# Performance work log

Measured on AMD Instinct MI355X. Metric: run time of the kernel, lower is better.

Reference implementation:

```python
import jax, jax.numpy as jnp
import numpy as np

D_EMB = 1024
N_HEAD = 16
D_K = D_EMB // N_HEAD


def setup_inputs() -> dict:
    key = jax.random.key(0)
    ks = jax.random.split(key, 11)
    B, S = 2, 2048
    s = 1.0 / np.sqrt(D_EMB)
    inp = {
        'Q': jax.random.normal(ks[0], (B, S, D_EMB), jnp.float32),
        'K': jax.random.normal(ks[1], (B, S, D_EMB), jnp.float32),
        'V': jax.random.normal(ks[2], (B, S, D_EMB), jnp.float32),
        'W_Q': jax.random.normal(ks[3], (D_EMB, D_EMB), jnp.float32) * s,
        'b_Q': jax.random.normal(ks[4], (D_EMB,), jnp.float32) * s,
        'W_K': jax.random.normal(ks[5], (D_EMB, D_EMB), jnp.float32) * s,
        'b_K': jax.random.normal(ks[6], (D_EMB,), jnp.float32) * s,
        'W_V': jax.random.normal(ks[7], (D_EMB, D_EMB), jnp.float32) * s,
        'b_V': jax.random.normal(ks[8], (D_EMB,), jnp.float32) * s,
        'W_O': jax.random.normal(ks[9], (D_EMB, D_EMB), jnp.float32) * s,
        'b_O': jax.random.normal(ks[10], (D_EMB,), jnp.float32) * s,
    }
    return inp


def _heads(x):
    # [B, S, D] -> [B, H, S, d_k]
    B, S, _ = x.shape
    return x.reshape(B, S, N_HEAD, D_K).transpose(0, 2, 1, 3)


def reference(Q, K, V, W_Q, b_Q, W_K, b_K, W_V, b_V, W_O, b_O):
    q = _heads(Q @ W_Q.T + b_Q)
    k = _heads(K @ W_K.T + b_K)
    v = _heads(V @ W_V.T + b_V)
    scale = 1.0 / jnp.sqrt(jnp.asarray(D_K, q.dtype))
    scores = jnp.einsum('bhqd,bhkd->bhqk', q, k) * scale  # [B,H,S,S]
    probs = jax.nn.softmax(scores, axis=-1)
    attn = jnp.einsum('bhqk,bhkd->bhqd', probs, v)
    B, H, S, d = attn.shape
    attn = attn.transpose(0, 2, 1, 3).reshape(B, S, H * d)
    return attn @ W_O.T + b_O
```

## Files before the change

### kernel.cpp

```cpp
#include <hip/hip_runtime.h>
#include <cstdint>
#include <cstddef>

#define S_LEN 2048
#define NH    16
#define DKH   64
#define DEMB  1024
#define MTOT  4096

typedef float f32x4 __attribute__((ext_vector_type(4)));
typedef __bf16 bf16x8 __attribute__((ext_vector_type(8)));
typedef unsigned short u16;
typedef unsigned int u32;
typedef u16 u16x8 __attribute__((ext_vector_type(8)));
typedef u16 u16x4 __attribute__((ext_vector_type(4)));
typedef u32 u32x2 __attribute__((ext_vector_type(2)));

static __device__ __forceinline__ u16 f2bf(float f) {
  u32 u = __builtin_bit_cast(u32, f);
  u += 0x7fffu + ((u >> 16) & 1u);
  return (u16)(u >> 16);
}
static __device__ __forceinline__ float bf2f(u16 b) {
  return __builtin_bit_cast(float, ((u32)b) << 16);
}
static __device__ __forceinline__ bf16x8 ldfrag(const u16* p) {
  return __builtin_bit_cast(bf16x8, *(const u16x8*)p);
}
static __device__ __forceinline__ f32x4 mfma16(bf16x8 a, bf16x8 b, f32x4 c) {
  return __builtin_amdgcn_mfma_f32_16x16x32_bf16(a, b, c, 0, 0, 0);
}
static __device__ __forceinline__ void gl2lds16(const void* g, void* l) {
  __builtin_amdgcn_global_load_lds((__attribute__((address_space(1))) void*)g,
                                   (__attribute__((address_space(3))) void*)l,
                                   16, 0, 0);
}
static __device__ __forceinline__ u32 pkbf(float hi, float lo) {
  u32 a = __builtin_bit_cast(u32, hi) + 0x8000u;
  u32 b = __builtin_bit_cast(u32, lo) + 0x8000u;
  return __builtin_amdgcn_perm(a, b, 0x07060302u);
}

#define SCL_Q (0.125f * 1.44269504088896340736f)

__global__ __launch_bounds__(256) void cvt_bf16(const float* __restrict__ s,
                                                u16* __restrict__ d, int n) {
  int i = (blockIdx.x * 256 + threadIdx.x) * 4;
  if (i >= n) return;
  f32x4 f = *(const f32x4*)(s + i);
  u16x4 o;
  o[0] = f2bf(f[0]); o[1] = f2bf(f[1]); o[2] = f2bf(f[2]); o[3] = f2bf(f[3]);
  *(u16x4*)(d + i) = o;
}

__global__ __launch_bounds__(256) void qkv_gemm(
    const u16* __restrict__ qin, const u16* __restrict__ kin,
    const u16* __restrict__ vin, const u16* __restrict__ W,
    const float* __restrict__ bq, const float* __restrict__ bk,
    const float* __restrict__ bv,
    u16* __restrict__ qh, u16* __restrict__ kh, u16* __restrict__ vt) {
  __shared__ __align__(16) u16 sA[128 * 32];
  __shared__ __align__(16) u16 sB[128 * 32];
  const int t = threadIdx.x;
  const int l = t & 63, w = t >> 6;
  const int ll = l & 15, lg = l >> 4;
  const int nb = blockIdx.x;
  const int mb = blockIdx.y;
  const int which = nb >> 3;
  const u16* A = (which == 0) ? qin : ((which == 1) ? kin : vin);
  const int wr = (w >> 1) * 64, wc = (w & 1) * 64;

  f32x4 acc[4][4] = {};

  for (int kt = 0; kt < 32; ++kt) {
    const int k0 = kt * 32;
    __syncthreads();
#pragma unroll
    for (int i = 0; i < 2; ++i) {
      const int c = i * 256 + t;
      const int row = c >> 2;
      const int gc = (c & 3) ^ ((row >> 1) & 3);
      gl2lds16(A + (size_t)(mb * 128 + row) * DEMB + k0 + gc * 8, &sA[c * 8]);
      gl2lds16(W + (size_t)(nb * 128 + row) * DEMB + k0 + gc * 8, &sB[c * 8]);
    }
    __syncthreads();

    bf16x8 af[4], bfr[4];
#pragma unroll
    for (int i2 = 0; i2 < 4; ++i2) {
      const int row = wr + i2 * 16 + ll;
      af[i2] = ldfrag(&sA[row * 32 + (lg ^ ((row >> 1) & 3)) * 8]);
    }
#pragma unroll
    for (int j2 = 0; j2 < 4; ++j2) {
      const int row = wc + j2 * 16 + ll;
      bfr[j2] = ldfrag(&sB[row * 32 + (lg ^ ((row >> 1) & 3)) * 8]);
    }
#pragma unroll
    for (int i2 = 0; i2 < 4; ++i2)
#pragma unroll
      for (int j2 = 0; j2 < 4; ++j2)
        acc[i2][j2] = mfma16(af[i2], bfr[j2], acc[i2][j2]);
  }

  const float* bias = (which == 0) ? bq : ((which == 1) ? bk : bv);
  const int b = (mb * 128) >> 11;

  if (which == 2) {
#pragma unroll
    for (int j2 = 0; j2 < 4; ++j2) {
      const int nl = (nb * 128 + wc + j2 * 16 + ll) & 1023;
      const int h = nl >> 6, dk = nl & 63;
      const float bb = bias[nl];
      u16* base = vt + ((size_t)((b * NH + h) * DKH + dk)) * S_LEN;
#pragma unroll
      for (int i2 = 0; i2 < 4; ++i2) {
        const int s = (mb * 128 + wr + i2 * 16 + lg * 4) & 2047;
        u16x4 pk;
#pragma unroll
        for (int r = 0; r < 4; ++r) pk[r] = f2bf(acc[i2][j2][r] + bb);
        *(u16x4*)&base[s] = pk;
      }
    }
  } else {
    u16* outp = (which == 0) ? qh : kh;
    const float scl = (which == 0) ? SCL_Q : 1.0f;
#pragma unroll
    for (int j2 = 0; j2 < 4; ++j2) {
      const int nl = (nb * 128 + wc + j2 * 16 + ll) & 1023;
      const int h = nl >> 6, dk = nl & 63;
      const float bb = bias[nl];
#pragma unroll
      for (int i2 = 0; i2 < 4; ++i2) {
#pragma unroll
        for (int r = 0; r < 4; ++r) {
          const int s = (mb * 128 + wr + i2 * 16 + lg * 4 + r) & 2047;
          const float val = (acc[i2][j2][r] + bb) * scl;
          outp[((size_t)((b * NH + h) * S_LEN + s)) * DKH + dk] = f2bf(val);
        }
      }
    }
  }
}

__global__ __launch_bounds__(256) void attn_kernel(
    const u16* __restrict__ qh, const u16* __restrict__ kh,
    const u16* __restrict__ vt, u16* __restrict__ opart,
    float* __restrict__ lpart) {
  __shared__ __align__(16) u16 sK[64 * 64];
  __shared__ __align__(16) u16 sV[64 * 64];
  __shared__ __align__(16) u16 sP[4][2][16 * 68];
  const int t = threadIdx.x;
  const int l = t & 63, w = t >> 6;
  const int ll = l & 15, lg = l >> 4;
  const int qb = blockIdx.x >> 1;
  const int ks = blockIdx.x & 1;
  const int q_blk = qb * 128;
  const int bh = blockIdx.y;

  bf16x8 aq[2][2];
#pragma unroll
  for (int qt = 0; qt < 2; ++qt) {
    const u16* qbase = qh + ((size_t)bh * S_LEN + q_blk + w * 32 + qt * 16 + ll) * DKH;
    aq[qt][0] = ldfrag(qbase + lg * 8);
    aq[qt][1] = ldfrag(qbase + 32 + lg * 8);
  }

  f32x4 oT[2][4] = {};
  float l_part[2] = {0.f, 0.f};

  u16* sP0 = &sP[w][0][0];
  u16* sP1 = &sP[w][1][0];

  for (int kt = 0; kt < 16; ++kt) {
    const int kb0 = ks * 1024 + kt * 64;
    __syncthreads();
#pragma unroll
    for (int i = 0; i < 2; ++i) {
      const int c = i * 256 + t;
      const int row = c >> 3, gc = (c & 7) ^ (row & 7);
      gl2lds16(kh + ((size_t)bh * S_LEN + kb0 + row) * DKH + gc * 8,
               &sK[c * 8]);
      gl2lds16(vt + ((size_t)bh * DKH + row) * S_LEN + kb0 + gc * 8,
               &sV[c * 8]);
    }
    __syncthreads();

#pragma unroll
    for (int kbl = 0; kbl < 4; ++kbl) {
      const int krow = kbl * 16 + ll;
      const bf16x8 ak0 = ldfrag(&sK[krow * 64 + (lg ^ (ll & 7)) * 8]);
      const bf16x8 ak1 = ldfrag(&sK[krow * 64 + ((4 + lg) ^ (ll & 7)) * 8]);
      f32x4 s0 = {}, s1 = {};
      s0 = mfma16(ak0, aq[0][0], s0);
      s0 = mfma16(ak1, aq[0][1], s0);
      s1 = mfma16(ak0, aq[1][0], s1);
      s1 = mfma16(ak1, aq[1][1], s1);
      const int poff = ll * 68 + kbl * 16 + lg * 4;
      {
        const float p0 = __builtin_amdgcn_exp2f(s0[0]);
        const float p1 = __builtin_amdgcn_exp2f(s0[1]);
        const float p2 = __builtin_amdgcn_exp2f(s0[2]);
        const float p3 = __builtin_amdgcn_exp2f(s0[3]);
        l_part[0] += (p0 + p1) + (p2 + p3);
        u32x2 pk; pk[0] = pkbf(p1, p0); pk[1] = pkbf(p3, p2);
        *(u32x2*)&sP0[poff] = pk;
      }
      {
        const float p0 = __builtin_amdgcn_exp2f(s1[0]);
        const float p1 = __builtin_amdgcn_exp2f(s1[1]);
        const float p2 = __builtin_amdgcn_exp2f(s1[2]);
        const float p3 = __builtin_amdgcn_exp2f(s1[3]);
        l_part[1] += (p0 + p1) + (p2 + p3);
        u32x2 pk; pk[0] = pkbf(p1, p0); pk[1] = pkbf(p3, p2);
        *(u32x2*)&sP1[poff] = pk;
      }
    }

    bf16x8 bp[2][2];
#pragma unroll
    for (int fl = 0; fl < 2; ++fl) {
      const int off = ll * 68 + fl * 32 + lg * 8;
      const u16x4 lo0 = *(const u16x4*)&sP0[off];
      const u16x4 hi0 = *(const u16x4*)&sP0[off + 4];
      bp[0][fl] = __builtin_bit_cast(bf16x8,
          __builtin_shufflevector(lo0, hi0, 0, 1, 2, 3, 4, 5, 6, 7));
      const u16x4 lo1 = *(const u16x4*)&sP1[off];
      const u16x4 hi1 = *(const u16x4*)&sP1[off + 4];
      bp[1][fl] = __builtin_bit_cast(bf16x8,
          __builtin_shufflevector(lo1, hi1, 0, 1, 2, 3, 4, 5, 6, 7));
    }
#pragma unroll
    for (int nt = 0; nt < 4; ++nt) {
      const int vrow = nt * 16 + ll;
#pragma unroll
      for (int fl = 0; fl < 2; ++fl) {
        const bf16x8 av = ldfrag(&sV[vrow * 64 + ((fl * 4 + lg) ^ (vrow & 7)) * 8]);
        oT[0][nt] = mfma16(av, bp[0][fl], oT[0][nt]);
        oT[1][nt] = mfma16(av, bp[1][fl], oT[1][nt]);
      }
    }
  }

#pragma unroll
  for (int qt = 0; qt < 2; ++qt) {
    float lv = l_part[qt];
    lv += __shfl_xor(lv, 16, 64);
    lv += __shfl_xor(lv, 32, 64);
    const int srow = q_blk + w * 32 + qt * 16 + ll;
    u16* obase = opart + (((size_t)(ks * 32 + bh)) * S_LEN + srow) * DKH;
#pragma unroll
    for (int nt = 0; nt < 4; ++nt) {
      u16x4 o;
#pragma unroll
      for (int r = 0; r < 4; ++r) o[r] = f2bf(oT[qt][nt][r]);
      *(u16x4*)&obase[nt * 16 + lg * 4] = o;
    }
    if (lg == 0) lpart[(ks * 32 + bh) * S_LEN + srow] = lv;
  }
}

__global__ __launch_bounds__(256) void merge_ctx(
    const u16* __restrict__ op, const float* __restrict__ lp,
    u16* __restrict__ ctx) {
  const int idx = blockIdx.x * 256 + threadIdx.x;
  const int dk8 = idx & 7;
  const int q = (idx >> 3) & 2047;
  const int bh = idx >> 14;
  const float inv = 1.0f / (lp[bh * S_LEN + q] + lp[(32 + bh) * S_LEN + q]);
  const u16x8 a = *(const u16x8*)&op[((size_t)bh * S_LEN + q) * DKH + dk8 * 8];
  const u16x8 c = *(const u16x8*)&op[((size_t)(32 + bh) * S_LEN + q) * DKH + dk8 * 8];
  u16x8 o;
#pragma unroll
  for (int r = 0; r < 8; ++r) o[r] = f2bf((bf2f(a[r]) + bf2f(c[r])) * inv);
  const int b = bh >> 4, h = bh & 15;
  *(u16x8*)&ctx[((size_t)((b * S_LEN + q) * NH + h)) * DKH + dk8 * 8] = o;
}

__global__ __launch_bounds__(256) void out_gemm(
    const u16* __restrict__ Am, const u16* __restrict__ W,
    const float* __restrict__ bo, float* __restrict__ out) {
  __shared__ __align__(16) u16 sA[64 * 64];
  __shared__ __align__(16) u16 sB[64 * 64];
  const int t = threadIdx.x;
  const int l = t & 63, w = t >> 6;
  const int ll = l & 15, lg = l >> 4;
  const int nb = blockIdx.x;
  const int mb = blockIdx.y;
  const int wr = (w >> 1) * 32, wc = (w & 1) * 32;

  f32x4 acc[2][2] = {};
  for (int kt = 0; kt < 16; ++kt) {
    const int k0 = kt * 64;
    __syncthreads();
#pragma unroll
    for (int i = 0; i < 2; ++i) {
      const int c = i * 256 + t;
      const int row = c >> 3;
      const int gc = (c & 7) ^ (row & 7);
      gl2lds16(Am + (size_t)(mb * 64 + row) * DEMB + k0 + gc * 8, &sA[c * 8]);
      gl2lds16(W + (size_t)(nb * 64 + row) * DEMB + k0 + gc * 8, &sB[c * 8]);
    }
    __syncthreads();
#pragma unroll
    for (int sub = 0; sub < 2; ++sub) {
      bf16x8 af[2], bfr[2];
#pragma unroll
      for (int i2 = 0; i2 < 2; ++i2) {
        const int row = wr + i2 * 16 + ll;
        af[i2] = ldfrag(&sA[row * 64 + ((sub * 4 + lg) ^ (row & 7)) * 8]);
      }
#pragma unroll
      for (int j2 = 0; j2 < 2; ++j2) {
        const int row = wc + j2 * 16 + ll;
        bfr[j2] = ldfrag(&sB[row * 64 + ((sub * 4 + lg) ^ (row & 7)) * 8]);
      }
#pragma unroll
      for (int i2 = 0; i2 < 2; ++i2)
#pragma unroll
        for (int j2 = 0; j2 < 2; ++j2)
          acc[i2][j2] = mfma16(af[i2], bfr[j2], acc[i2][j2]);
    }
  }

#pragma unroll
  for (int j2 = 0; j2 < 2; ++j2) {
    const int ncol = nb * 64 + wc + j2 * 16 + ll;
    const float bb = bo[ncol];
#pragma unroll
    for (int i2 = 0; i2 < 2; ++i2) {
#pragma unroll
      for (int r = 0; r < 4; ++r) {
        const int mrow = mb * 64 + wr + i2 * 16 + lg * 4 + r;
        out[(size_t)mrow * DEMB + ncol] = acc[i2][j2][r] + bb;
      }
    }
  }
}

extern "C" void kernel_launch(void* const* d_in, const int* in_sizes, int n_in,
                              void* d_out, int out_size, void* d_ws,
                              size_t ws_size, hipStream_t stream) {
  (void)in_sizes; (void)n_in; (void)out_size; (void)ws_size;
  const float* Q  = (const float*)d_in[0];
  const float* K  = (const float*)d_in[1];
  const float* V  = (const float*)d_in[2];
  const float* WQ = (const float*)d_in[3];
  const float* bQ = (const float*)d_in[4];
  const float* WK = (const float*)d_in[5];
  const float* bK = (const float*)d_in[6];
  const float* WV = (const float*)d_in[7];
  const float* bV = (const float*)d_in[8];
  const float* WO = (const float*)d_in[9];
  const float* bO = (const float*)d_in[10];
  float* out = (float*)d_out;

  u16* ws   = (u16*)d_ws;
  u16* Wqkv = ws;
  u16* Wo   = Wqkv + 3072 * 1024;
  u16* qin  = Wo + 1024 * 1024;
  u16* kin  = qin + (size_t)MTOT * DEMB;
  u16* vin  = kin + (size_t)MTOT * DEMB;
  u16* qh   = vin + (size_t)MTOT * DEMB;
  u16* kh   = qh + 32 * 2048 * 64;
  u16* vt   = kh + 32 * 2048 * 64;
  u16* ctx  = vt + 32 * 2048 * 64;
  u16* opart   = qin;
  float* lpart = (float*)Wqkv;

  const int WN = DEMB * DEMB;
  const int AN = MTOT * DEMB;
  cvt_bf16<<<WN / 1024, 256, 0, stream>>>(WQ, Wqkv, WN);
  cvt_bf16<<<WN / 1024, 256, 0, stream>>>(WK, Wqkv + WN, WN);
  cvt_bf16<<<WN / 1024, 256, 0, stream>>>(WV, Wqkv + 2 * WN, WN);
  cvt_bf16<<<WN / 1024, 256, 0, stream>>>(WO, Wo, WN);
  cvt_bf16<<<AN / 1024, 256, 0, stream>>>(Q, qin, AN);
  cvt_bf16<<<AN / 1024, 256, 0, stream>>>(K, kin, AN);
  cvt_bf16<<<AN / 1024, 256, 0, stream>>>(V, vin, AN);

  qkv_gemm<<<dim3(24, 32), 256, 0, stream>>>(qin, kin, vin, Wqkv, bQ, bK, bV,
                                             qh, kh, vt);
  attn_kernel<<<dim3(32, 32), 256, 0, stream>>>(qh, kh, vt, opart, lpart);
  merge_ctx<<<2048, 256, 0, stream>>>(opart, lpart, ctx);
  out_gemm<<<dim3(16, 64), 256, 0, stream>>>(ctx, Wo, bO, out);
}
```

Before: 251.3 us.

## Keep P in registers via fp16 16x16x16 MFMA and merge conversion launches

The attention kernel no longer writes the softmax probabilities to LDS and reads them back. It packs them to fp16 in registers and feeds them directly as the B operand of 16x16x16 f16 MFMAs, since that instruction's accumulator layout matches its input layout. V is now stored as fp16 so the PV product runs in f16, which removes the LDS round trip and its latency, at the cost of twice as many smaller MFMAs. Separately, the seven fp32-to-bf16 conversion launches are merged into one kernel to cut launch overhead. Using fp16 for V and P changes rounding, and the range of V must fit in fp16.

```diff
diff --git a/kernel.cpp b/kernel.cpp
--- a/kernel.cpp
+++ b/kernel.cpp
@@ -10,11 +10,13 @@
 
 typedef float f32x4 __attribute__((ext_vector_type(4)));
 typedef __bf16 bf16x8 __attribute__((ext_vector_type(8)));
+typedef _Float16 f16;
+typedef f16 f16x2 __attribute__((ext_vector_type(2)));
+typedef f16 f16x4 __attribute__((ext_vector_type(4)));
 typedef unsigned short u16;
 typedef unsigned int u32;
 typedef u16 u16x8 __attribute__((ext_vector_type(8)));
 typedef u16 u16x4 __attribute__((ext_vector_type(4)));
-typedef u32 u32x2 __attribute__((ext_vector_type(2)));
 
 static __device__ __forceinline__ u16 f2bf(float f) {
   u32 u = __builtin_bit_cast(u32, f);
@@ -27,26 +29,48 @@
 static __device__ __forceinline__ bf16x8 ldfrag(const u16* p) {
   return __builtin_bit_cast(bf16x8, *(const u16x8*)p);
 }
+static __device__ __forceinline__ f16x4 ldfragh(const u16* p) {
+  return __builtin_bit_cast(f16x4, *(const u16x4*)p);
+}
 static __device__ __forceinline__ f32x4 mfma16(bf16x8 a, bf16x8 b, f32x4 c) {
   return __builtin_amdgcn_mfma_f32_16x16x32_bf16(a, b, c, 0, 0, 0);
+}
+static __device__ __forceinline__ f32x4 mfmah(f16x4 a, f16x4 b, f32x4 c) {
+  return __builtin_amdgcn_mfma_f32_16x16x16f16(a, b, c, 0, 0, 0);
 }
 static __device__ __forceinline__ void gl2lds16(const void* g, void* l) {
   __builtin_amdgcn_global_load_lds((__attribute__((address_space(1))) void*)g,
                                    (__attribute__((address_space(3))) void*)l,
                                    16, 0, 0);
 }
-static __device__ __forceinline__ u32 pkbf(float hi, float lo) {
-  u32 a = __builtin_bit_cast(u32, hi) + 0x8000u;
-  u32 b = __builtin_bit_cast(u32, lo) + 0x8000u;
-  return __builtin_amdgcn_perm(a, b, 0x07060302u);
+static __device__ __forceinline__ f16x4 pkh4(float a, float b, float c, float d) {
+  f16x2 lo = __builtin_bit_cast(f16x2, __builtin_amdgcn_cvt_pkrtz(a, b));
+  f16x2 hi = __builtin_bit_cast(f16x2, __builtin_amdgcn_cvt_pkrtz(c, d));
+  return __builtin_shufflevector(lo, hi, 0, 1, 2, 3);
 }
 
 #define SCL_Q (0.125f * 1.44269504088896340736f)
 
-__global__ __launch_bounds__(256) void cvt_bf16(const float* __restrict__ s,
-                                                u16* __restrict__ d, int n) {
-  int i = (blockIdx.x * 256 + threadIdx.x) * 4;
-  if (i >= n) return;
+__global__ __launch_bounds__(256) void cvt_all(
+    const float* __restrict__ wq, const float* __restrict__ wk,
+    const float* __restrict__ wv, const float* __restrict__ wo,
+    const float* __restrict__ q, const float* __restrict__ k,
+    const float* __restrict__ v, u16* __restrict__ dW, u16* __restrict__ dA) {
+  int b = blockIdx.x;
+  const float* s; u16* d;
+  if (b < 4096) {
+    const int seg = b >> 10;
+    s = (seg == 0) ? wq : (seg == 1) ? wk : (seg == 2) ? wv : wo;
+    d = dW + (size_t)seg * (DEMB * DEMB);
+    b &= 1023;
+  } else {
+    const int bb = b - 4096;
+    const int seg = bb >> 12;
+    s = (seg == 0) ? q : (seg == 1) ? k : v;
+    d = dA + (size_t)seg * ((size_t)MTOT * DEMB);
+    b = bb & 4095;
+  }
+  const int i = (b * 256 + threadIdx.x) * 4;
   f32x4 f = *(const f32x4*)(s + i);
   u16x4 o;
   o[0] = f2bf(f[0]); o[1] = f2bf(f[1]); o[2] = f2bf(f[2]); o[3] = f2bf(f[3]);
@@ -116,10 +140,9 @@
 #pragma unroll
       for (int i2 = 0; i2 < 4; ++i2) {
         const int s = (mb * 128 + wr + i2 * 16 + lg * 4) & 2047;
-        u16x4 pk;
-#pragma unroll
-        for (int r = 0; r < 4; ++r) pk[r] = f2bf(acc[i2][j2][r] + bb);
-        *(u16x4*)&base[s] = pk;
+        const f16x4 pk = pkh4(acc[i2][j2][0] + bb, acc[i2][j2][1] + bb,
+                              acc[i2][j2][2] + bb, acc[i2][j2][3] + bb);
+        *(u16x4*)&base[s] = __builtin_bit_cast(u16x4, pk);
       }
     }
   } else {
@@ -149,7 +172,6 @@
     float* __restrict__ lpart) {
   __shared__ __align__(16) u16 sK[64 * 64];
   __shared__ __align__(16) u16 sV[64 * 64];
-  __shared__ __align__(16) u16 sP[4][2][16 * 68];
   const int t = threadIdx.x;
   const int l = t & 63, w = t >> 6;
   const int ll = l & 15, lg = l >> 4;
@@ -168,9 +190,6 @@
 
   f32x4 oT[2][4] = {};
   float l_part[2] = {0.f, 0.f};
-
-  u16* sP0 = &sP[w][0][0];
-  u16* sP1 = &sP[w][1][0];
 
   for (int kt = 0; kt < 16; ++kt) {
     const int kb0 = ks * 1024 + kt * 64;
@@ -196,15 +215,15 @@
       s0 = mfma16(ak1, aq[0][1], s0);
       s1 = mfma16(ak0, aq[1][0], s1);
       s1 = mfma16(ak1, aq[1][1], s1);
-      const int poff = ll * 68 + kbl * 16 + lg * 4;
+
+      f16x4 bp0, bp1;
       {
         const float p0 = __builtin_amdgcn_exp2f(s0[0]);
         const float p1 = __builtin_amdgcn_exp2f(s0[1]);
         const float p2 = __builtin_amdgcn_exp2f(s0[2]);
         const float p3 = __builtin_amdgcn_exp2f(s0[3]);
         l_part[0] += (p0 + p1) + (p2 + p3);
-        u32x2 pk; pk[0] = pkbf(p1, p0); pk[1] = pkbf(p3, p2);
-        *(u32x2*)&sP0[poff] = pk;
+        bp0 = pkh4(p0, p1, p2, p3);
       }
       {
         const float p0 = __builtin_amdgcn_exp2f(s1[0]);
@@ -212,32 +231,16 @@
         const float p2 = __builtin_amdgcn_exp2f(s1[2]);
         const float p3 = __builtin_amdgcn_exp2f(s1[3]);
         l_part[1] += (p0 + p1) + (p2 + p3);
-        u32x2 pk; pk[0] = pkbf(p1, p0); pk[1] = pkbf(p3, p2);
-        *(u32x2*)&sP1[poff] = pk;
-      }
-    }
-
-    bf16x8 bp[2][2];
-#pragma unroll
-    for (int fl = 0; fl < 2; ++fl) {
-      const int off = ll * 68 + fl * 32 + lg * 8;
-      const u16x4 lo0 = *(const u16x4*)&sP0[off];
-      const u16x4 hi0 = *(const u16x4*)&sP0[off + 4];
-      bp[0][fl] = __builtin_bit_cast(bf16x8,
-          __builtin_shufflevector(lo0, hi0, 0, 1, 2, 3, 4, 5, 6, 7));
-      const u16x4 lo1 = *(const u16x4*)&sP1[off];
-      const u16x4 hi1 = *(const u16x4*)&sP1[off + 4];
-      bp[1][fl] = __builtin_bit_cast(bf16x8,
-          __builtin_shufflevector(lo1, hi1, 0, 1, 2, 3, 4, 5, 6, 7));
-    }
-#pragma unroll
-    for (int nt = 0; nt < 4; ++nt) {
-      const int vrow = nt * 16 + ll;
-#pragma unroll
-      for (int fl = 0; fl < 2; ++fl) {
-        const bf16x8 av = ldfrag(&sV[vrow * 64 + ((fl * 4 + lg) ^ (vrow & 7)) * 8]);
-        oT[0][nt] = mfma16(av, bp[0][fl], oT[0][nt]);
-        oT[1][nt] = mfma16(av, bp[1][fl], oT[1][nt]);
+        bp1 = pkh4(p0, p1, p2, p3);
+      }
+
+#pragma unroll
+      for (int nt = 0; nt < 4; ++nt) {
+        const int row = nt * 16 + ll;
+        const int ch = (kbl * 2 + (lg >> 1)) ^ (ll & 7);
+        const f16x4 av = ldfragh(&sV[row * 64 + ch * 8 + (lg & 1) * 4]);
+        oT[0][nt] = mfmah(av, bp0, oT[0][nt]);
+        oT[1][nt] = mfmah(av, bp1, oT[1][nt]);
       }
     }
   }
@@ -368,15 +371,7 @@
   u16* opart   = qin;
   float* lpart = (float*)Wqkv;
 
-  const int WN = DEMB * DEMB;
-  const int AN = MTOT * DEMB;
-  cvt_bf16<<<WN / 1024, 256, 0, stream>>>(WQ, Wqkv, WN);
-  cvt_bf16<<<WN / 1024, 256, 0, stream>>>(WK, Wqkv + WN, WN);
-  cvt_bf16<<<WN / 1024, 256, 0, stream>>>(WV, Wqkv + 2 * WN, WN);
-  cvt_bf16<<<WN / 1024, 256, 0, stream>>>(WO, Wo, WN);
-  cvt_bf16<<<AN / 1024, 256, 0, stream>>>(Q, qin, AN);
-  cvt_bf16<<<AN / 1024, 256, 0, stream>>>(K, kin, AN);
-  cvt_bf16<<<AN / 1024, 256, 0, stream>>>(V, vin, AN);
+  cvt_all<<<16384, 256, 0, stream>>>(WQ, WK, WV, WO, Q, K, V, Wqkv, qin);
 
   qkv_gemm<<<dim3(24, 32), 256, 0, stream>>>(qin, kin, vin, Wqkv, bQ, bK, bV,
                                              qh, kh, vt);
```

Result: faster. 239.0 us (-4.9%).
